# Kernel tuning notes

Measured on AMD Instinct MI355X. Metric: run time of the kernel, lower is better.

## Reference

```python
import jax, jax.numpy as jnp
import numpy as np

SUPPORT = 7
NEIGHBOR = 10
EPS = 1e-12
BN_EPS = 1e-5


def knn(v, k):
    # v: (b, n, 3) -> (b, n, k) indices of k nearest (excluding self)
    sq = jnp.sum(v * v, -1)
    d = sq[:, :, None] + sq[:, None, :] - 2.0 * jnp.einsum('bnd,bmd->bnm', v, v)
    _, idx = jax.lax.top_k(-d, k + 1)
    return idx[:, :, 1:]


def gather_nb(f, idx):
    # f: (b, n, c), idx: (b, m, k) -> (b, m, k, c)
    b = f.shape[0]
    return f[jnp.arange(b)[:, None, None], idx]


def nb_dir_norm(v, idx):
    d = gather_nb(v, idx) - v[:, :, None, :]
    n = jnp.linalg.norm(d, axis=-1, keepdims=True)
    return d / jnp.maximum(n, EPS)


def norm0(d):
    n = jnp.linalg.norm(d, axis=0, keepdims=True)
    return d / jnp.maximum(n, EPS)


def conv_surface(idx, v, directions, kernel_num):
    b, n, k = idx.shape
    dn = nb_dir_norm(v, idx)
    theta = jax.nn.relu(jnp.einsum('bnkd,de->bnke', dn, norm0(directions)))
    theta = theta.reshape(b, n, k, SUPPORT, kernel_num)
    return jnp.sum(jnp.max(theta, axis=2), axis=2)  # (b, n, kernel_num)


def conv_layer(idx, v, fmap, w, bias, directions, out_ch):
    b, n, k = idx.shape
    dn = nb_dir_norm(v, idx)
    theta = jax.nn.relu(jnp.einsum('bnkd,de->bnke', dn, norm0(directions)))  # (b,n,k,s*o)
    fout = fmap @ w + bias  # (b, n, (s+1)*o)
    center = fout[..., :out_ch]
    supp = gather_nb(fout[..., out_ch:], idx)  # (b, n, k, s*o)
    act = (theta * supp).reshape(b, n, k, SUPPORT, out_ch)
    return center + jnp.sum(jnp.max(act, axis=2), axis=2)


def pool(v, f, rate, nbn, seed):
    b, n, _ = v.shape
    idx = knn(v, nbn)
    pf = jnp.max(gather_nb(f, idx), axis=2)
    m = n // rate
    samp = jax.random.permutation(jax.random.key(seed), n)[:m]
    return v[:, samp, :], pf[:, samp, :]


def nearest_idx(tgt, src):
    d = (jnp.sum(src * src, -1)[:, None, :] + jnp.sum(tgt * tgt, -1)[:, :, None]
         - 2.0 * jnp.einsum('btd,bsd->bts', tgt, src))
    return jnp.argmin(d, axis=-1)  # (b, nt)


def bn(x, g, b_, m, var):
    # per-channel over last dim (torch BN1d after transpose)
    return (x - m) / jnp.sqrt(var + BN_EPS) * g + b_


def setup_inputs() -> dict:
    key = jax.random.key(0)
    ks = jax.random.split(key, 32)
    bs, n = 4, 2048
    d = {}
    d['vertices'] = jax.random.normal(ks[0], (bs, n, 3), jnp.float32)
    d['rgb_f'] = jax.random.normal(ks[1], (bs, 32, n), jnp.float32)
    d['dir0'] = jax.random.normal(ks[2], (3, SUPPORT * 64), jnp.float32)
    def conv_params(i, cin, cout):
        s = 1.0 / np.sqrt(cin)
        w = jax.random.uniform(ks[i], (cin, (SUPPORT + 1) * cout), jnp.float32, -s, s)
        b = jax.random.uniform(ks[i + 1], ((SUPPORT + 1) * cout,), jnp.float32, -s, s)
        dr = jax.random.normal(ks[i + 2], (3, SUPPORT * cout), jnp.float32)
        return w, b, dr
    d['w1'], d['b1'], d['d1'] = conv_params(3, 128, 128)
    d['w2'], d['b2'], d['d2'] = conv_params(6, 128, 256)
    d['w3'], d['b3'], d['d3'] = conv_params(9, 256, 256)
    d['w4'], d['b4'], d['d4'] = conv_params(12, 256, 512)
    d['rgb_w'] = jax.random.normal(ks[15], (64, 32), jnp.float32) * 0.1
    d['rgb_b'] = jnp.zeros((64,), jnp.float32)
    for nm, c in [('rbn', 64), ('bn1', 128), ('bn2', 256), ('bn3', 256)]:
        d[nm + '_g'] = jnp.ones((c,), jnp.float32)
        d[nm + '_b'] = jnp.zeros((c,), jnp.float32)
        d[nm + '_m'] = jnp.zeros((c,), jnp.float32)
        d[nm + '_v'] = jnp.ones((c,), jnp.float32)
    return d


def reference(vertices, rgb_f, dir0,
              w1, b1, d1, w2, b2, d2, w3, b3, d3, w4, b4, d4,
              rgb_w, rgb_b,
              rbn_g, rbn_b, rbn_m, rbn_v,
              bn1_g, bn1_b, bn1_m, bn1_v,
              bn2_g, bn2_b, bn2_m, bn2_v,
              bn3_g, bn3_b, bn3_m, bn3_v):
    bs, n, _ = vertices.shape
    idx = knn(vertices, NEIGHBOR)
    fm0 = jax.nn.relu(conv_surface(idx, vertices, dir0, 64))  # (b, n, 64)
    # rgb_conv_1: Conv1d(32,64,1) -> ReLU -> BN
    rgb = jax.nn.relu(jnp.einsum('oc,bcn->bno', rgb_w, rgb_f) + rgb_b)  # (b, n, 64)
    rgb = bn(rgb, rbn_g, rbn_b, rbn_m, rbn_v)
    fm0 = jnp.concatenate([fm0, rgb], axis=-1)  # (b, n, 128)
    fm1 = jax.nn.relu(bn(conv_layer(idx, vertices, fm0, w1, b1, d1, 128),
                         bn1_g, bn1_b, bn1_m, bn1_v))
    v1, fp1 = pool(vertices, fm1, 4, 4, 1)  # (b, n/4, ...)
    k1 = min(NEIGHBOR, v1.shape[1] // 8)
    idx1 = knn(v1, k1)
    fm2 = jax.nn.relu(bn(conv_layer(idx1, v1, fp1, w2, b2, d2, 256),
                         bn2_g, bn2_b, bn2_m, bn2_v))
    fm3 = jax.nn.relu(bn(conv_layer(idx1, v1, fm2, w3, b3, d3, 256),
                         bn3_g, bn3_b, bn3_m, bn3_v))
    v2, fp2 = pool(v1, fm3, 4, 4, 2)  # (b, n/16, ...)
    k2 = min(NEIGHBOR, v2.shape[1] // 8)
    idx2 = knn(v2, k2)
    fm4 = conv_layer(idx2, v2, fp2, w4, b4, d4, 512)
    f_global = jnp.max(fm4, axis=1)  # (b, 512)
    ni1 = nearest_idx(vertices, v1)  # (b, n)
    ni2 = nearest_idx(vertices, v2)
    ar = jnp.arange(bs)[:, None]
    fm2u = fm2[ar, ni1]
    fm3u = fm3[ar, ni1]
    fm4u = fm4[ar, ni2]
    feat = jnp.concatenate([fm0, fm1, fm2u, fm3u, fm4u], axis=2)  # (b, n, 1280)
    fuse = jnp.concatenate([feat, jnp.broadcast_to(f_global[:, None, :], (bs, n, 512))], axis=2)
    return feat.transpose(0, 2, 1), fuse.transpose(0, 2, 1)
```

## Files before the change

### kernel.cpp

```cpp
#include <hip/hip_runtime.h>
#include <hip/hip_bf16.h>
#include <math.h>

#define NB 10
#define KNN_K 11

typedef __attribute__((ext_vector_type(8))) short bf16x8;
typedef __attribute__((ext_vector_type(4))) float f32x4;
typedef unsigned long long ull;

__device__ __forceinline__ float toF(float x) { return x; }
__device__ __forceinline__ float toF(__hip_bfloat16 x) { return __bfloat162float(x); }

__device__ __forceinline__ void tf2x32(unsigned k0, unsigned k1, unsigned& x0, unsigned& x1) {
  unsigned ks0 = k0, ks1 = k1, ks2 = k0 ^ k1 ^ 0x1BD11BDAu;
  x0 += ks0; x1 += ks1;
#define TF_R(r) { x0 += x1; x1 = (x1 << (r)) | (x1 >> (32 - (r))); x1 ^= x0; }
  TF_R(13) TF_R(15) TF_R(26) TF_R(6)  x0 += ks1; x1 += ks2 + 1u;
  TF_R(17) TF_R(29) TF_R(16) TF_R(24) x0 += ks2; x1 += ks0 + 2u;
  TF_R(13) TF_R(15) TF_R(26) TF_R(6)  x0 += ks0; x1 += ks1 + 3u;
  TF_R(17) TF_R(29) TF_R(16) TF_R(24) x0 += ks1; x1 += ks2 + 4u;
  TF_R(13) TF_R(15) TF_R(26) TF_R(6)  x0 += ks2; x1 += ks0 + 5u;
#undef TF_R
}

template <int NITER>
__device__ __forceinline__ void knn_extract_body(const float4* __restrict__ pts, int qi,
                                                 int lane, int* __restrict__ o) {
  float4 p = pts[qi];
  float d[NITER];
#pragma unroll
  for (int i = 0; i < NITER; ++i) {
    float4 q = pts[lane + 64 * i];
    float dot = p.x * q.x + p.y * q.y + p.z * q.z;
    d[i] = p.w + q.w - 2.0f * dot;
  }
  unsigned mask = 0u;
#pragma unroll 1
  for (int t = 0; t < KNN_K; ++t) {
    float bestd = 3.4e38f; int besti = 0x7fffffff;
#pragma unroll
    for (int i = 0; i < NITER; ++i) {
      bool valid = ((mask >> i) & 1u) == 0u;
      bool better = valid && (d[i] < bestd);
      bestd = better ? d[i] : bestd;
      besti = better ? (lane + 64 * i) : besti;
    }
    float rd = bestd; int ridx = besti;
#pragma unroll
    for (int s = 32; s > 0; s >>= 1) {
      float od = __shfl_xor(rd, s);
      int oi = __shfl_xor(ridx, s);
      if (od < rd || (od == rd && oi < ridx)) { rd = od; ridx = oi; }
    }
    if ((ridx & 63) == lane) mask |= 1u << (ridx >> 6);
    if (t >= 1 && lane == 0) o[t - 1] = ridx;
  }
}

template <int NITER>
__global__ __launch_bounds__(1024) void knn_wave_kernel(const float* __restrict__ v,
                                                        int* __restrict__ out) {
  __shared__ float4 pts[NITER * 64];
  const int N = NITER * 64;
  int b = blockIdx.y;
  const float* vb = v + (size_t)b * N * 3;
  for (int i = threadIdx.x; i < N; i += blockDim.x) {
    float x = vb[i * 3], y = vb[i * 3 + 1], z = vb[i * 3 + 2];
    pts[i] = make_float4(x, y, z, x * x + y * y + z * z);
  }
  __syncthreads();
  int qpb = blockDim.x >> 6;
  int wave = threadIdx.x >> 6;
  int lane = threadIdx.x & 63;
  int qi = blockIdx.x * qpb + wave;
  knn_extract_body<NITER>(pts, qi, lane, out + ((size_t)b * N + qi) * NB);
}

__global__ __launch_bounds__(1024) void prep_kernel(
    const float* __restrict__ w1, __hip_bfloat16* __restrict__ o1,
    const float* __restrict__ w2, __hip_bfloat16* __restrict__ o2,
    const float* __restrict__ w3, __hip_bfloat16* __restrict__ o3,
    const float* __restrict__ w4, __hip_bfloat16* __restrict__ o4,
    const float* __restrict__ s0, float* __restrict__ n0,
    const float* __restrict__ s1, float* __restrict__ n1,
    const float* __restrict__ s2, float* __restrict__ n2,
    const float* __restrict__ s3, float* __restrict__ n3,
    const float* __restrict__ s4, float* __restrict__ n4,
    int* __restrict__ p1a, int* __restrict__ p1b, int* __restrict__ samp2) {
  __shared__ __align__(16) char smem[16896];
  int bid = blockIdx.x;
  if (bid < 480) {
    int sub = threadIdx.x >> 8, t = threadIdx.x & 255;
    int wtile = bid * 4 + sub;
    float (*tbuf)[33] = (float(*)[33])(smem + sub * (32 * 33 * 4));
    const float* W; __hip_bfloat16* O; int K, N;
    if (wtile < 128)      { W = w1; O = o1; K = 128; N = 1024; }
    else if (wtile < 384) { wtile -= 128; W = w2; O = o2; K = 128; N = 2048; }
    else if (wtile < 896) { wtile -= 384; W = w3; O = o3; K = 256; N = 2048; }
    else                  { wtile -= 896; W = w4; O = o4; K = 256; N = 4096; }
    int tpr = N / 32;
    int tk = wtile / tpr, tn = wtile % tpr;
    int tx = t & 31, ty = t >> 5;
#pragma unroll
    for (int i = 0; i < 4; ++i)
      tbuf[ty + 8 * i][tx] = W[(size_t)(tk * 32 + ty + 8 * i) * N + tn * 32 + tx];
    __syncthreads();
#pragma unroll
    for (int i = 0; i < 4; ++i)
      O[(size_t)(tn * 32 + ty + 8 * i) * K + tk * 32 + tx] = __float2bfloat16(tbuf[tx][ty + 8 * i]);
    return;
  }
  if (bid < 489) {
    int e = (bid - 480) * 1024 + threadIdx.x;
    const float* S; float* D; int W;
    if (e < 448)                          { S = s0; D = n0; W = 448; }
    else if (e < 448 + 896)               { e -= 448; S = s1; D = n1; W = 896; }
    else if (e < 448 + 896 + 1792)        { e -= 448 + 896; S = s2; D = n2; W = 1792; }
    else if (e < 448 + 896 + 3584)        { e -= 448 + 896 + 1792; S = s3; D = n3; W = 1792; }
    else if (e < 448 + 896 + 3584 + 3584) { e -= 448 + 896 + 3584; S = s4; D = n4; W = 3584; }
    else return;
    float a = S[e], b = S[W + e], c = S[2 * W + e];
    float nr = fmaxf(sqrtf(a * a + b * b + c * c), 1e-12f);
    D[e] = a / nr; D[W + e] = b / nr; D[2 * W + e] = c / nr;
    return;
  }
  {
    ull* keys = (ull*)smem;
    int which, chunk;
    if (bid < 497)      { which = 0; chunk = bid - 489; }
    else if (bid < 505) { which = 1; chunk = bid - 497; }
    else                { which = 2; chunk = 0; }
    unsigned mk0, mk1;
    if (which == 0)      { mk0 = 0u; mk1 = 1u; }
    else if (which == 1) { unsigned a0 = 0u, a1 = 0u; tf2x32(0u, 1u, a0, a1); mk0 = a0; mk1 = a1; }
    else                 { mk0 = 0u; mk1 = 2u; }
    unsigned sk0 = 0u, sk1 = 1u;
    tf2x32(mk0, mk1, sk0, sk1);
    int n = (which == 2) ? 512 : 2048;
    int* outp = (which == 0) ? p1a : (which == 1) ? p1b : samp2;
    for (int i = threadIdx.x; i < n; i += 1024) {
      unsigned y0 = 0u, y1 = (unsigned)i;
      tf2x32(sk0, sk1, y0, y1);
      keys[i] = ((ull)(y0 ^ y1) << 32) | (unsigned)i;
    }
    __syncthreads();
    int rpb = (which == 2) ? 512 : 256;
    int tpr = 1024 / rpb;
    int row = chunk * rpb + (int)(threadIdx.x / tpr);
    int sub = threadIdx.x % tpr;
    int seg = n / tpr;
    ull my = keys[row];
    int cnt = 0;
    for (int j = sub * seg; j < (sub + 1) * seg; ++j) cnt += (keys[j] < my) ? 1 : 0;
#pragma unroll
    for (int m = 1; m < 4; m <<= 1)
      if (m < tpr) cnt += __shfl_xor(cnt, m);
    if (sub == 0) outp[cnt] = row;
  }
}

__global__ __launch_bounds__(256) void fm0n_kernel(const float* __restrict__ v, const int* __restrict__ idx,
                                                   const float* __restrict__ dir0n,
                                                   const float* __restrict__ rgb_f, const float* __restrict__ w,
                                                   const float* __restrict__ bias, const float* __restrict__ g,
                                                   const float* __restrict__ bb, const float* __restrict__ mm,
                                                   const float* __restrict__ vv,
                                                   const int* __restrict__ p1a, const int* __restrict__ p1b,
                                                   const int* __restrict__ samp2,
                                                   float* __restrict__ fm0, __hip_bfloat16* __restrict__ fm0b,
                                                   int* __restrict__ ni1, int* __restrict__ ni2) {
  int z = blockIdx.z;
  int b = blockIdx.y;
  int tid = threadIdx.x;
  if (z >= 1) {
    __shared__ float4 sp[512];
    int S = (z == 1) ? 512 : 128;
    int* outp = (z == 1) ? ni1 : ni2;
    for (int i = tid; i < S; i += blockDim.x) {
      int src = (z == 1) ? p1a[p1b[i]] : p1a[p1b[samp2[i]]];
      const float* q = v + ((size_t)b * 2048 + src) * 3;
      float x = q[0], y = q[1], zz = q[2];
      sp[i] = make_float4(x, y, zz, x * x + y * y + zz * zz);
    }
    __syncthreads();
    int wave = tid >> 6, lane = tid & 63;
    int n = blockIdx.x * 4 + wave;
    const float* t = v + ((size_t)b * 2048 + n) * 3;
    float x = t[0], y = t[1], zz = t[2];
    float sqt = x * x + y * y + zz * zz;
    float best = 3.4e38f; int bi = 0x7fffffff;
    for (int s = lane; s < S; s += 64) {
      float4 q = sp[s];
      float d = q.w + sqt - 2.f * (x * q.x + y * q.y + zz * q.z);
      if (d < best) { best = d; bi = s; }
    }
#pragma unroll
    for (int m = 32; m > 0; m >>= 1) {
      float od = __shfl_xor(best, m);
      int oi = __shfl_xor(bi, m);
      if (od < best || (od == best && oi < bi)) { best = od; bi = oi; }
    }
    if (lane == 0) outp[(size_t)b * 2048 + n] = bi;
    return;
  }
  __shared__ float dn[4][NB][3];
  int n0 = blockIdx.x * 4;
  if (tid < 4 * NB) {
    int p = tid / NB, k = tid % NB;
    size_t row = (size_t)b * 2048 + (n0 + p);
    const float* c = v + row * 3;
    int nb = idx[row * NB + k];
    const float* q = v + ((size_t)b * 2048 + nb) * 3;
    float dx = q[0] - c[0], dy = q[1] - c[1], dz = q[2] - c[2];
    float nr = fmaxf(sqrtf(dx * dx + dy * dy + dz * dz), 1e-12f);
    dn[p][k][0] = dx / nr; dn[p][k][1] = dy / nr; dn[p][k][2] = dz / nr;
  }
  __syncthreads();
  int p = tid >> 6, c = tid & 63;
  int n = n0 + p;
  float acc = 0.f;
  for (int s = 0; s < 7; ++s) {
    int e = s * 64 + c;
    float d0 = dir0n[e], d1 = dir0n[448 + e], d2 = dir0n[896 + e];
    float mx = 0.f;
#pragma unroll
    for (int k = 0; k < NB; ++k) {
      float t = dn[p][k][0] * d0 + dn[p][k][1] * d1 + dn[p][k][2] * d2;
      mx = fmaxf(mx, fmaxf(t, 0.f));
    }
    acc += mx;
  }
  acc = fmaxf(acc, 0.f);
  const float* f = rgb_f + (size_t)b * 32 * 2048;
  float a2 = bias[c];
  for (int cc = 0; cc < 32; ++cc) a2 += w[c * 32 + cc] * f[cc * 2048 + n];
  a2 = fmaxf(a2, 0.f);
  a2 = (a2 - mm[c]) / sqrtf(vv[c] + 1e-5f) * g[c] + bb[c];
  size_t o = ((size_t)b * 2048 + n) * 128;
  fm0[o + c] = acc;
  fm0[o + 64 + c] = a2;
  fm0b[o + c] = __float2bfloat16(acc);
  fm0b[o + 64 + c] = __float2bfloat16(a2);
}

__global__ __launch_bounds__(256) void mfma_gemm_kernel(const __hip_bfloat16* __restrict__ A,
                                                        const __hip_bfloat16* __restrict__ BT,
                                                        const float* __restrict__ bias,
                                                        float* __restrict__ C,
                                                        __hip_bfloat16* __restrict__ Cb,
                                                        int M, int K, int N) {
  __shared__ __hip_bfloat16 Al[128 * 32];
  __shared__ __hip_bfloat16 Bl[128 * 32];
  int t = threadIdx.x;
  int l = t & 63;
  int w = t >> 6;
  int wm = w >> 1, wn = w & 1;
  int m0 = blockIdx.y * 128, n0 = blockIdx.x * 128;
  f32x4 zero = {0.f, 0.f, 0.f, 0.f};
  f32x4 acc[4][4];
#pragma unroll
  for (int i = 0; i < 4; ++i)
#pragma unroll
    for (int j = 0; j < 4; ++j) acc[i][j] = zero;

  for (int kt = 0; kt < K; kt += 32) {
#pragma unroll
    for (int j = 0; j < 2; ++j) {
      int c = t + 256 * j;
      int r = c >> 2, o = c & 3;
      *(uint4*)&Al[r * 32 + o * 8] = *(const uint4*)&A[(size_t)(m0 + r) * K + kt + o * 8];
      *(uint4*)&Bl[r * 32 + o * 8] = *(const uint4*)&BT[(size_t)(n0 + r) * K + kt + o * 8];
    }
    __syncthreads();
    bf16x8 af[4], bfv[4];
#pragma unroll
    for (int f = 0; f < 4; ++f) {
      af[f]  = *(const bf16x8*)&Al[(wm * 64 + f * 16 + (l & 15)) * 32 + (l >> 4) * 8];
      bfv[f] = *(const bf16x8*)&Bl[(wn * 64 + f * 16 + (l & 15)) * 32 + (l >> 4) * 8];
    }
#pragma unroll
    for (int i = 0; i < 4; ++i)
#pragma unroll
      for (int j = 0; j < 4; ++j)
        acc[i][j] = __builtin_amdgcn_mfma_f32_16x16x32_bf16(af[i], bfv[j], acc[i][j], 0, 0, 0);
    __syncthreads();
  }
  int col_l = l & 15, rbase = (l >> 4) * 4;
#pragma unroll
  for (int i = 0; i < 4; ++i) {
#pragma unroll
    for (int j = 0; j < 4; ++j) {
      int col = n0 + wn * 64 + j * 16 + col_l;
      float bv = bias[col];
#pragma unroll
      for (int r = 0; r < 4; ++r) {
        int m = m0 + wm * 64 + i * 16 + rbase + r;
        float val = acc[i][j][r] + bv;
        if (C)  C[(size_t)m * N + col] = val;
        if (Cb) Cb[(size_t)m * N + col] = __float2bfloat16(val);
      }
    }
  }
}

template <typename T>
__global__ __launch_bounds__(256) void conv_combine3_kernel(
    const int* __restrict__ idx, const float* __restrict__ v,
    const T* __restrict__ fout, const float* __restrict__ dirn,
    const float* __restrict__ g, const float* __restrict__ bb,
    const float* __restrict__ mm, const float* __restrict__ vv,
    int use_bn_relu, float* __restrict__ outf, __hip_bfloat16* __restrict__ outb,
    int Np, int Cout) {
  __shared__ float dnS[2][NB][3];
  __shared__ int nbS[2][NB];
  int b = blockIdx.y;
  int tid = threadIdx.x;
  int base = blockIdx.x * 256;
  int p0 = base / Cout;
  int nPts = (Cout < 256) ? 2 : 1;
  if (tid < nPts * NB) {
    int p = tid / NB, k = tid - p * NB;
    size_t prow = (size_t)b * Np + p0 + p;
    int nb = idx[prow * NB + k];
    const float* cpt = v + prow * 3;
    const float* q = v + ((size_t)b * Np + nb) * 3;
    float dx = q[0] - cpt[0], dy = q[1] - cpt[1], dz = q[2] - cpt[2];
    float nr = fmaxf(sqrtf(dx * dx + dy * dy + dz * dz), 1e-12f);
    dnS[p][k][0] = dx / nr; dnS[p][k][1] = dy / nr; dnS[p][k][2] = dz / nr;
    nbS[p][k] = b * Np + nb;
  }
  __syncthreads();
  int gid = base + tid;
  int n = gid / Cout, c = gid - n * Cout;
  int lp = n - p0;
  size_t row = (size_t)b * Np + n;
  float dn0[NB], dn1[NB], dn2[NB]; int nbr[NB];
#pragma unroll
  for (int k = 0; k < NB; ++k) {
    dn0[k] = dnS[lp][k][0]; dn1[k] = dnS[lp][k][1]; dn2[k] = dnS[lp][k][2];
    nbr[k] = nbS[lp][k];
  }
  int F = 8 * Cout, W7 = 7 * Cout;
  float acc = toF(fout[row * (size_t)F + c]);
  for (int s = 0; s < 7; ++s) {
    int e = s * Cout + c;
    float d0 = dirn[e], d1 = dirn[W7 + e], d2 = dirn[2 * W7 + e];
    float mx = -3.4e38f;
#pragma unroll
    for (int k = 0; k < NB; ++k) {
      float t = fmaxf(dn0[k] * d0 + dn1[k] * d1 + dn2[k] * d2, 0.f);
      float sv = toF(fout[(size_t)nbr[k] * F + Cout + e]);
      mx = fmaxf(mx, t * sv);
    }
    acc += mx;
  }
  if (use_bn_relu) {
    acc = (acc - mm[c]) / sqrtf(vv[c] + 1e-5f) * g[c] + bb[c];
    acc = fmaxf(acc, 0.f);
  }
  outf[row * (size_t)Cout + c] = acc;
  if (outb) outb[row * (size_t)Cout + c] = __float2bfloat16(acc);
}

__global__ void pool_kernel(const float* __restrict__ v, const float* __restrict__ fm,
                            const int* __restrict__ idx10,
                            const int* __restrict__ sampA, const int* __restrict__ sampB,
                            float* __restrict__ v_out, float* __restrict__ f_out,
                            __hip_bfloat16* __restrict__ f_out_b, int Nin, int C) {
  int b = blockIdx.y, mi = blockIdx.x, c = threadIdx.x;
  int n = sampB ? sampA[sampB[mi]] : sampA[mi];
  size_t row = (size_t)b * Nin + n;
  float mx = -3.4e38f;
#pragma unroll
  for (int j = 0; j < 4; ++j) {
    int nb = idx10[row * NB + j];
    mx = fmaxf(mx, fm[((size_t)b * Nin + nb) * C + c]);
  }
  int Mout = gridDim.x;
  f_out[((size_t)b * Mout + mi) * C + c] = mx;
  f_out_b[((size_t)b * Mout + mi) * C + c] = __float2bfloat16(mx);
  if (c < 3) v_out[((size_t)b * Mout + mi) * 3 + c] = v[row * 3 + c];
}

__global__ __launch_bounds__(256) void output3_kernel(
    const float* __restrict__ fm0, const float* __restrict__ fm1,
    const float* __restrict__ fm2, const float* __restrict__ fm3,
    const float* __restrict__ fm4,
    const int* __restrict__ ni1, const int* __restrict__ ni2,
    float* __restrict__ out) {
  __shared__ float tile[64][33];
  __shared__ int srow[64];
  int b = blockIdx.z;
  int cc0 = blockIdx.y * 32;
  int n0 = blockIdx.x * 64;
  int tid = threadIdx.x;
  float* out0 = out;
  float* out1 = out + (size_t)4 * 1280 * 2048;
  if (cc0 >= 1280) {
    __shared__ float red[8][32];
    __shared__ float fgv[32];
    int coff = cc0 - 1280;
    int tx = tid & 31, ty = tid >> 5;
    float pm = -3.4e38f;
    for (int p = ty; p < 128; p += 8)
      pm = fmaxf(pm, fm4[((size_t)b * 128 + p) * 512 + coff + tx]);
    red[ty][tx] = pm;
    __syncthreads();
    if (tid < 32) {
      float m = red[0][tid];
#pragma unroll
      for (int r = 1; r < 8; ++r) m = fmaxf(m, red[r][tid]);
      fgv[tid] = m;
    }
    __syncthreads();
    int lx = tid & 63, ly = tid >> 6;
#pragma unroll
    for (int ci = 0; ci < 8; ++ci) {
      int cl = ly + 4 * ci;
      out1[((size_t)b * 1792 + cc0 + cl) * 2048 + n0 + lx] = fgv[cl];
    }
    return;
  }
  const float* P; int Cs, coff, mode;
  if (cc0 < 128)       { P = fm0; Cs = 128; coff = cc0;        mode = 0; }
  else if (cc0 < 256)  { P = fm1; Cs = 128; coff = cc0 - 128;  mode = 0; }
  else if (cc0 < 512)  { P = fm2; Cs = 256; coff = cc0 - 256;  mode = 1; }
  else if (cc0 < 768)  { P = fm3; Cs = 256; coff = cc0 - 512;  mode = 1; }
  else                 { P = fm4; Cs = 512; coff = cc0 - 768;  mode = 2; }
  if (tid < 64) {
    int n = n0 + tid;
    size_t r2 = (size_t)b * 2048 + n;
    int sr;
    if (mode == 0)      sr = b * 2048 + n;
    else if (mode == 1) sr = b * 512 + ni1[r2];
    else                sr = b * 128 + ni2[r2];
    srow[tid] = sr;
  }
  __syncthreads();
  int tx = tid & 31, ty = tid >> 5;
#pragma unroll
  for (int r = 0; r < 8; ++r) {
    int nl = ty + 8 * r;
    tile[nl][tx] = P[(size_t)srow[nl] * Cs + coff + tx];
  }
  __syncthreads();
  int lx = tid & 63, ly = tid >> 6;
#pragma unroll
  for (int ci = 0; ci < 8; ++ci) {
    int cl = ly + 4 * ci;
    int cc = cc0 + cl;
    float vv = tile[lx][cl];
    out1[((size_t)b * 1792 + cc) * 2048 + n0 + lx] = vv;
    out0[((size_t)b * 1280 + cc) * 2048 + n0 + lx] = vv;
  }
}

extern "C" void kernel_launch(void* const* d_in, const int* in_sizes, int n_in,
                              void* d_out, int out_size, void* d_ws, size_t ws_size,
                              hipStream_t stream) {
  (void)in_sizes; (void)n_in; (void)out_size; (void)ws_size;
  const float* vertices = (const float*)d_in[0];
  const float* rgb_f    = (const float*)d_in[1];
  const float* dir0     = (const float*)d_in[2];
  const float* w1 = (const float*)d_in[3],  *b1 = (const float*)d_in[4],  *d1 = (const float*)d_in[5];
  const float* w2 = (const float*)d_in[6],  *b2 = (const float*)d_in[7],  *d2 = (const float*)d_in[8];
  const float* w3 = (const float*)d_in[9],  *b3 = (const float*)d_in[10], *d3 = (const float*)d_in[11];
  const float* w4 = (const float*)d_in[12], *b4 = (const float*)d_in[13], *d4 = (const float*)d_in[14];
  const float* rgb_w = (const float*)d_in[15], *rgb_b = (const float*)d_in[16];
  const float* rbn_g = (const float*)d_in[17], *rbn_b = (const float*)d_in[18];
  const float* rbn_m = (const float*)d_in[19], *rbn_v = (const float*)d_in[20];
  const float* bn1_g = (const float*)d_in[21], *bn1_b = (const float*)d_in[22];
  const float* bn1_m = (const float*)d_in[23], *bn1_v = (const float*)d_in[24];
  const float* bn2_g = (const float*)d_in[25], *bn2_b = (const float*)d_in[26];
  const float* bn2_m = (const float*)d_in[27], *bn2_v = (const float*)d_in[28];
  const float* bn3_g = (const float*)d_in[29], *bn3_b = (const float*)d_in[30];
  const float* bn3_m = (const float*)d_in[31], *bn3_v = (const float*)d_in[32];
  float* out = (float*)d_out;

  char* ws = (char*)d_ws;
  size_t off = 0;
  auto alloc = [&](size_t bytes) -> void* {
    void* p = ws + off;
    off += (bytes + 255) & ~(size_t)255;
    return p;
  };
  int*   p1a   = (int*)alloc(2048 * 4);
  int*   p1b   = (int*)alloc(2048 * 4);
  int*   samp2 = (int*)alloc(512 * 4);
  int*   idx0  = (int*)alloc((size_t)4 * 2048 * NB * 4);
  int*   idx1  = (int*)alloc((size_t)4 * 512 * NB * 4);
  int*   idx2  = (int*)alloc((size_t)4 * 128 * NB * 4);
  float* fm0   = (float*)alloc((size_t)4 * 2048 * 128 * 4);
  float* fm1   = (float*)alloc((size_t)4 * 2048 * 128 * 4);
  float* fout  = (float*)alloc((size_t)4 * 2048 * 1024 * 4);
  __hip_bfloat16* foutb = (__hip_bfloat16*)alloc((size_t)4 * 2048 * 1024 * 2);
  float* v1    = (float*)alloc((size_t)4 * 512 * 3 * 4);
  float* fp1   = (float*)alloc((size_t)4 * 512 * 128 * 4);
  float* fm2   = (float*)alloc((size_t)4 * 512 * 256 * 4);
  float* fm3   = (float*)alloc((size_t)4 * 512 * 256 * 4);
  float* v2    = (float*)alloc((size_t)4 * 128 * 3 * 4);
  float* fp2   = (float*)alloc((size_t)4 * 128 * 256 * 4);
  float* fm4   = (float*)alloc((size_t)4 * 128 * 512 * 4);
  int*   ni1   = (int*)alloc((size_t)4 * 2048 * 4);
  int*   ni2   = (int*)alloc((size_t)4 * 2048 * 4);
  __hip_bfloat16* fm0b = (__hip_bfloat16*)alloc((size_t)4 * 2048 * 128 * 2);
  __hip_bfloat16* fp1b = (__hip_bfloat16*)alloc((size_t)4 * 512 * 128 * 2);
  __hip_bfloat16* fm2b = (__hip_bfloat16*)alloc((size_t)4 * 512 * 256 * 2);
  __hip_bfloat16* fp2b = (__hip_bfloat16*)alloc((size_t)4 * 128 * 256 * 2);
  __hip_bfloat16* wt1  = (__hip_bfloat16*)alloc((size_t)1024 * 128 * 2);
  __hip_bfloat16* wt2  = (__hip_bfloat16*)alloc((size_t)2048 * 128 * 2);
  __hip_bfloat16* wt3  = (__hip_bfloat16*)alloc((size_t)2048 * 256 * 2);
  __hip_bfloat16* wt4  = (__hip_bfloat16*)alloc((size_t)4096 * 256 * 2);
  float* d0n = (float*)alloc((size_t)3 * 448 * 4);
  float* d1n = (float*)alloc((size_t)3 * 896 * 4);
  float* d2n = (float*)alloc((size_t)3 * 1792 * 4);
  float* d3n = (float*)alloc((size_t)3 * 1792 * 4);
  float* d4n = (float*)alloc((size_t)3 * 3584 * 4);

  prep_kernel<<<506, 1024, 0, stream>>>(w1, wt1, w2, wt2, w3, wt3, w4, wt4,
                                        dir0, d0n, d1, d1n, d2, d2n, d3, d3n, d4, d4n,
                                        p1a, p1b, samp2);

  knn_wave_kernel<32><<<dim3(128, 4), 1024, 0, stream>>>(vertices, idx0);

  fm0n_kernel<<<dim3(512, 4, 3), 256, 0, stream>>>(vertices, idx0, d0n, rgb_f, rgb_w, rgb_b,
                                                   rbn_g, rbn_b, rbn_m, rbn_v, p1a, p1b, samp2,
                                                   fm0, fm0b, ni1, ni2);

  mfma_gemm_kernel<<<dim3(1024 / 128, 8192 / 128), 256, 0, stream>>>(fm0b, wt1, b1, nullptr, foutb, 8192, 128, 1024);
  conv_combine3_kernel<__hip_bfloat16><<<dim3(2048 * 128 / 256, 4), 256, 0, stream>>>(idx0, vertices, foutb, d1n,
      bn1_g, bn1_b, bn1_m, bn1_v, 1, fm1, nullptr, 2048, 128);

  pool_kernel<<<dim3(512, 4), 128, 0, stream>>>(vertices, fm1, idx0, p1a, p1b, v1, fp1, fp1b, 2048, 128);
  knn_wave_kernel<8><<<dim3(128, 4), 256, 0, stream>>>(v1, idx1);

  mfma_gemm_kernel<<<dim3(2048 / 128, 2048 / 128), 256, 0, stream>>>(fp1b, wt2, b2, nullptr, foutb, 2048, 128, 2048);
  conv_combine3_kernel<__hip_bfloat16><<<dim3(512 * 256 / 256, 4), 256, 0, stream>>>(idx1, v1, foutb, d2n,
      bn2_g, bn2_b, bn2_m, bn2_v, 1, fm2, fm2b, 512, 256);
  mfma_gemm_kernel<<<dim3(2048 / 128, 2048 / 128), 256, 0, stream>>>(fm2b, wt3, b3, nullptr, foutb, 2048, 256, 2048);
  conv_combine3_kernel<__hip_bfloat16><<<dim3(512 * 256 / 256, 4), 256, 0, stream>>>(idx1, v1, foutb, d3n,
      bn3_g, bn3_b, bn3_m, bn3_v, 1, fm3, nullptr, 512, 256);

  pool_kernel<<<dim3(128, 4), 256, 0, stream>>>(v1, fm3, idx1, samp2, nullptr, v2, fp2, fp2b, 512, 256);
  knn_wave_kernel<2><<<dim3(32, 4), 256, 0, stream>>>(v2, idx2);

  mfma_gemm_kernel<<<dim3(4096 / 128, 512 / 128), 256, 0, stream>>>(fp2b, wt4, b4, fout, nullptr, 512, 256, 4096);
  conv_combine3_kernel<float><<<dim3(128 * 512 / 256, 4), 256, 0, stream>>>(idx2, v2, fout, d4n,
      nullptr, nullptr, nullptr, nullptr, 0, fm4, nullptr, 128, 512);

  output3_kernel<<<dim3(32, 56, 4), 256, 0, stream>>>(fm0, fm1, fm2, fm3, fm4, ni1, ni2, out);
}
```

Measured before the change: 252.6 us.

## Replace wave-per-query KNN with thread-per-query split top-k and merge

The first-level KNN over 2048 points used to run one wavefront per query, doing 11 rounds of wave-wide argmin shuffles. It now runs one thread per query: each thread keeps a register insertion-sorted top-11 over a 256-point slice, and a second kernel merges the 8 partial lists per query. The partial results are staged in the existing fout scratch buffer, and the launch adds one extra kernel. Separately, the permutation-rank part of the prep kernel is spread over more blocks, with fewer rows per block and more threads counting each row, to raise parallelism.

```diff
diff --git a/kernel.cpp b/kernel.cpp
--- a/kernel.cpp
+++ b/kernel.cpp
@@ -24,6 +24,74 @@
 #undef TF_R
 }
 
+#define KNN_INSERT(cd_, ci_)                                 \
+  {                                                          \
+    float cdv_ = (cd_); int civ_ = (ci_);                    \
+    _Pragma("unroll")                                        \
+    for (int t_ = 0; t_ < KNN_K; ++t_) {                     \
+      bool sw_ = cdv_ < bd[t_];                              \
+      float td_ = bd[t_]; int ti_ = bi[t_];                  \
+      bd[t_] = sw_ ? cdv_ : td_; bi[t_] = sw_ ? civ_ : ti_;  \
+      cdv_ = sw_ ? td_ : cdv_;   civ_ = sw_ ? ti_ : civ_;    \
+    }                                                        \
+  }
+
+__global__ __launch_bounds__(256) void knn0_part_kernel(const float* __restrict__ v,
+                                                        float* __restrict__ partd,
+                                                        int* __restrict__ parti) {
+  __shared__ float4 pts[256];
+  int b = blockIdx.z, sl = blockIdx.y, qb = blockIdx.x;
+  const float* vb = v + (size_t)b * 2048 * 3;
+  int c0 = sl * 256;
+  {
+    int j = c0 + threadIdx.x;
+    float x = vb[j * 3], y = vb[j * 3 + 1], z = vb[j * 3 + 2];
+    pts[threadIdx.x] = make_float4(x, y, z, x * x + y * y + z * z);
+  }
+  __syncthreads();
+  int q = qb * 256 + threadIdx.x;
+  float px = vb[q * 3], py = vb[q * 3 + 1], pz = vb[q * 3 + 2];
+  float pw = px * px + py * py + pz * pz;
+  float bd[KNN_K]; int bi[KNN_K];
+#pragma unroll
+  for (int t = 0; t < KNN_K; ++t) { bd[t] = 3.4e38f; bi[t] = 0x7fffffff; }
+  for (int i = 0; i < 256; ++i) {
+    float4 qq = pts[i];
+    float dot = px * qq.x + py * qq.y + pz * qq.z;
+    float d = pw + qq.w - 2.0f * dot;
+    if (d < bd[KNN_K - 1]) KNN_INSERT(d, c0 + i);
+  }
+  size_t base = ((size_t)(b * 8 + sl) * KNN_K) * 2048 + q;
+#pragma unroll
+  for (int k = 0; k < KNN_K; ++k) {
+    partd[base + (size_t)k * 2048] = bd[k];
+    parti[base + (size_t)k * 2048] = bi[k];
+  }
+}
+
+__global__ __launch_bounds__(256) void knn0_merge_kernel(const float* __restrict__ partd,
+                                                         const int* __restrict__ parti,
+                                                         int* __restrict__ idx0) {
+  int b = blockIdx.y;
+  int q = blockIdx.x * 256 + threadIdx.x;
+  float bd[KNN_K]; int bi[KNN_K];
+#pragma unroll
+  for (int t = 0; t < KNN_K; ++t) { bd[t] = 3.4e38f; bi[t] = 0x7fffffff; }
+  for (int s = 0; s < 8; ++s) {
+    for (int k = 0; k < KNN_K; ++k) {
+      size_t base = ((size_t)(b * 8 + s) * KNN_K + k) * 2048 + q;
+      float cd = partd[base];
+      if (cd < bd[KNN_K - 1]) {
+        int ci = parti[base];
+        KNN_INSERT(cd, ci);
+      } else break;
+    }
+  }
+  int* o = idx0 + ((size_t)b * 2048 + q) * NB;
+#pragma unroll
+  for (int t = 1; t < KNN_K; ++t) o[t - 1] = bi[t];
+}
+
 template <int NITER>
 __device__ __forceinline__ void knn_extract_body(const float4* __restrict__ pts, int qi,
                                                  int lane, int* __restrict__ o) {
@@ -59,8 +127,7 @@
 }
 
 template <int NITER>
-__global__ __launch_bounds__(1024) void knn_wave_kernel(const float* __restrict__ v,
-                                                        int* __restrict__ out) {
+__global__ void knn_wave_kernel(const float* __restrict__ v, int* __restrict__ out) {
   __shared__ float4 pts[NITER * 64];
   const int N = NITER * 64;
   int b = blockIdx.y;
@@ -128,8 +195,8 @@
   {
     ull* keys = (ull*)smem;
     int which, chunk;
-    if (bid < 497)      { which = 0; chunk = bid - 489; }
-    else if (bid < 505) { which = 1; chunk = bid - 497; }
+    if (bid < 521)      { which = 0; chunk = bid - 489; }
+    else if (bid < 553) { which = 1; chunk = bid - 521; }
     else                { which = 2; chunk = 0; }
     unsigned mk0, mk1;
     if (which == 0)      { mk0 = 0u; mk1 = 1u; }
@@ -145,7 +212,7 @@
       keys[i] = ((ull)(y0 ^ y1) << 32) | (unsigned)i;
     }
     __syncthreads();
-    int rpb = (which == 2) ? 512 : 256;
+    int rpb = (which == 2) ? 512 : 64;
     int tpr = 1024 / rpb;
     int row = chunk * rpb + (int)(threadIdx.x / tpr);
     int sub = threadIdx.x % tpr;
@@ -154,7 +221,7 @@
     int cnt = 0;
     for (int j = sub * seg; j < (sub + 1) * seg; ++j) cnt += (keys[j] < my) ? 1 : 0;
 #pragma unroll
-    for (int m = 1; m < 4; m <<= 1)
+    for (int m = 1; m < 16; m <<= 1)
       if (m < tpr) cnt += __shfl_xor(cnt, m);
     if (sub == 0) outp[cnt] = row;
   }
@@ -518,11 +585,15 @@
   float* d3n = (float*)alloc((size_t)3 * 1792 * 4);
   float* d4n = (float*)alloc((size_t)3 * 3584 * 4);
 
-  prep_kernel<<<506, 1024, 0, stream>>>(w1, wt1, w2, wt2, w3, wt3, w4, wt4,
+  float* partd = fout;
+  int*   parti = (int*)(fout + 720896);
+
+  prep_kernel<<<554, 1024, 0, stream>>>(w1, wt1, w2, wt2, w3, wt3, w4, wt4,
                                         dir0, d0n, d1, d1n, d2, d2n, d3, d3n, d4, d4n,
                                         p1a, p1b, samp2);
 
-  knn_wave_kernel<32><<<dim3(128, 4), 1024, 0, stream>>>(vertices, idx0);
+  knn0_part_kernel<<<dim3(8, 8, 4), 256, 0, stream>>>(vertices, partd, parti);
+  knn0_merge_kernel<<<dim3(8, 4), 256, 0, stream>>>(partd, parti, idx0);
 
   fm0n_kernel<<<dim3(512, 4, 3), 256, 0, stream>>>(vertices, idx0, d0n, rgb_f, rgb_w, rgb_b,
                                                    rbn_g, rbn_b, rbn_m, rbn_v, p1a, p1b, samp2,
```

Result: slower. 406.1 us (+60.7%).

## Replace wave-per-query KNN with thread-per-query insertion sort and split-merge

Applied to the files above, without the earlier changes.

The wave-per-query KNN, which ran 11 rounds of wave reductions, is replaced by a per-thread register top-11 insertion sort. The large level-0 KNN is split across 16 candidate slices with partial results written to scratch memory that aliases fout, then merged in a second kernel. The small levels use a single thread-per-query kernel. The permutation-rank part of prep_kernel is also spread over more blocks (64 rows per block instead of 256). Risks include very low parallelism in knn_small (2 and 1 blocks per batch), divergence in the insert branch, and tie-breaking that may differ from top_k.

```diff
diff --git a/kernel.cpp b/kernel.cpp
--- a/kernel.cpp
+++ b/kernel.cpp
@@ -24,45 +24,78 @@
 #undef TF_R
 }
 
-template <int NITER>
-__device__ __forceinline__ void knn_extract_body(const float4* __restrict__ pts, int qi,
-                                                 int lane, int* __restrict__ o) {
-  float4 p = pts[qi];
-  float d[NITER];
-#pragma unroll
-  for (int i = 0; i < NITER; ++i) {
-    float4 q = pts[lane + 64 * i];
-    float dot = p.x * q.x + p.y * q.y + p.z * q.z;
-    d[i] = p.w + q.w - 2.0f * dot;
-  }
-  unsigned mask = 0u;
-#pragma unroll 1
-  for (int t = 0; t < KNN_K; ++t) {
-    float bestd = 3.4e38f; int besti = 0x7fffffff;
-#pragma unroll
-    for (int i = 0; i < NITER; ++i) {
-      bool valid = ((mask >> i) & 1u) == 0u;
-      bool better = valid && (d[i] < bestd);
-      bestd = better ? d[i] : bestd;
-      besti = better ? (lane + 64 * i) : besti;
-    }
-    float rd = bestd; int ridx = besti;
-#pragma unroll
-    for (int s = 32; s > 0; s >>= 1) {
-      float od = __shfl_xor(rd, s);
-      int oi = __shfl_xor(ridx, s);
-      if (od < rd || (od == rd && oi < ridx)) { rd = od; ridx = oi; }
-    }
-    if ((ridx & 63) == lane) mask |= 1u << (ridx >> 6);
-    if (t >= 1 && lane == 0) o[t - 1] = ridx;
-  }
-}
-
-template <int NITER>
-__global__ __launch_bounds__(1024) void knn_wave_kernel(const float* __restrict__ v,
+#define KNN_DECL                                                        \
+  float d0=3.4e38f,d1=3.4e38f,d2=3.4e38f,d3=3.4e38f,d4=3.4e38f,         \
+        d5=3.4e38f,d6=3.4e38f,d7=3.4e38f,d8=3.4e38f,d9=3.4e38f,d10=3.4e38f; \
+  int   i0=0x7fffffff,i1=0x7fffffff,i2=0x7fffffff,i3=0x7fffffff,        \
+        i4=0x7fffffff,i5=0x7fffffff,i6=0x7fffffff,i7=0x7fffffff,        \
+        i8=0x7fffffff,i9=0x7fffffff,i10=0x7fffffff;
+
+#define KNN_SLOT(K)                                                     \
+  { bool sw_ = cdv_ < d##K; float td_ = d##K; int ti_ = i##K;           \
+    d##K = sw_ ? cdv_ : td_; i##K = sw_ ? civ_ : ti_;                   \
+    cdv_ = sw_ ? td_ : cdv_; civ_ = sw_ ? ti_ : civ_; }
+
+#define KNN_INSERT_S(cd_, ci_)                                          \
+  { float cdv_ = (cd_); int civ_ = (ci_);                               \
+    KNN_SLOT(0) KNN_SLOT(1) KNN_SLOT(2) KNN_SLOT(3) KNN_SLOT(4)        \
+    KNN_SLOT(5) KNN_SLOT(6) KNN_SLOT(7) KNN_SLOT(8) KNN_SLOT(9)        \
+    KNN_SLOT(10) }
+
+__global__ __launch_bounds__(256) void knn0_part_kernel(const float* __restrict__ v,
+                                                        float* __restrict__ partd,
+                                                        int* __restrict__ parti) {
+  __shared__ float4 pts[128];
+  int b = blockIdx.z, sl = blockIdx.y, qb = blockIdx.x;
+  const float* vb = v + (size_t)b * 2048 * 3;
+  int c0 = sl * 128;
+  if (threadIdx.x < 128) {
+    int j = c0 + threadIdx.x;
+    float x = vb[j * 3], y = vb[j * 3 + 1], z = vb[j * 3 + 2];
+    pts[threadIdx.x] = make_float4(x, y, z, x * x + y * y + z * z);
+  }
+  __syncthreads();
+  int q = qb * 256 + threadIdx.x;
+  float px = vb[q * 3], py = vb[q * 3 + 1], pz = vb[q * 3 + 2];
+  float pw = px * px + py * py + pz * pz;
+  KNN_DECL
+  for (int i = 0; i < 128; ++i) {
+    float4 qq = pts[i];
+    float dot = px * qq.x + py * qq.y + pz * qq.z;
+    float d = pw + qq.w - 2.0f * dot;
+    if (d < d10) KNN_INSERT_S(d, c0 + i);
+  }
+  size_t base = ((size_t)(b * 16 + sl) * KNN_K) * 2048 + q;
+#define KNN_STORE(K) { partd[base + (size_t)K * 2048] = d##K; parti[base + (size_t)K * 2048] = i##K; }
+  KNN_STORE(0) KNN_STORE(1) KNN_STORE(2) KNN_STORE(3) KNN_STORE(4)
+  KNN_STORE(5) KNN_STORE(6) KNN_STORE(7) KNN_STORE(8) KNN_STORE(9) KNN_STORE(10)
+#undef KNN_STORE
+}
+
+__global__ __launch_bounds__(256) void knn0_merge_kernel(const float* __restrict__ partd,
+                                                         const int* __restrict__ parti,
+                                                         int* __restrict__ idx0) {
+  int b = blockIdx.y;
+  int q = blockIdx.x * 256 + threadIdx.x;
+  KNN_DECL
+  for (int s = 0; s < 16; ++s) {
+    for (int k = 0; k < KNN_K; ++k) {
+      size_t base = ((size_t)(b * 16 + s) * KNN_K + k) * 2048 + q;
+      float cd = partd[base];
+      if (cd < d10) {
+        int ci = parti[base];
+        KNN_INSERT_S(cd, ci);
+      } else break;
+    }
+  }
+  int* o = idx0 + ((size_t)b * 2048 + q) * NB;
+  o[0] = i1; o[1] = i2; o[2] = i3; o[3] = i4; o[4] = i5;
+  o[5] = i6; o[6] = i7; o[7] = i8; o[8] = i9; o[9] = i10;
+}
+
+__global__ __launch_bounds__(256) void knn_small_kernel(const float* __restrict__ v, int N,
                                                         int* __restrict__ out) {
-  __shared__ float4 pts[NITER * 64];
-  const int N = NITER * 64;
+  __shared__ float4 pts[512];
   int b = blockIdx.y;
   const float* vb = v + (size_t)b * N * 3;
   for (int i = threadIdx.x; i < N; i += blockDim.x) {
@@ -70,11 +103,19 @@
     pts[i] = make_float4(x, y, z, x * x + y * y + z * z);
   }
   __syncthreads();
-  int qpb = blockDim.x >> 6;
-  int wave = threadIdx.x >> 6;
-  int lane = threadIdx.x & 63;
-  int qi = blockIdx.x * qpb + wave;
-  knn_extract_body<NITER>(pts, qi, lane, out + ((size_t)b * N + qi) * NB);
+  int q = blockIdx.x * 256 + threadIdx.x;
+  if (q >= N) return;
+  float4 p = pts[q];
+  KNN_DECL
+  for (int i = 0; i < N; ++i) {
+    float4 qq = pts[i];
+    float dot = p.x * qq.x + p.y * qq.y + p.z * qq.z;
+    float d = p.w + qq.w - 2.0f * dot;
+    if (d < d10) KNN_INSERT_S(d, i);
+  }
+  int* o = out + ((size_t)b * N + q) * NB;
+  o[0] = i1; o[1] = i2; o[2] = i3; o[3] = i4; o[4] = i5;
+  o[5] = i6; o[6] = i7; o[7] = i8; o[8] = i9; o[9] = i10;
 }
 
 __global__ __launch_bounds__(1024) void prep_kernel(
@@ -128,8 +169,8 @@
   {
     ull* keys = (ull*)smem;
     int which, chunk;
-    if (bid < 497)      { which = 0; chunk = bid - 489; }
-    else if (bid < 505) { which = 1; chunk = bid - 497; }
+    if (bid < 521)      { which = 0; chunk = bid - 489; }
+    else if (bid < 553) { which = 1; chunk = bid - 521; }
     else                { which = 2; chunk = 0; }
     unsigned mk0, mk1;
     if (which == 0)      { mk0 = 0u; mk1 = 1u; }
@@ -145,7 +186,7 @@
       keys[i] = ((ull)(y0 ^ y1) << 32) | (unsigned)i;
     }
     __syncthreads();
-    int rpb = (which == 2) ? 512 : 256;
+    int rpb = (which == 2) ? 512 : 64;
     int tpr = 1024 / rpb;
     int row = chunk * rpb + (int)(threadIdx.x / tpr);
     int sub = threadIdx.x % tpr;
@@ -154,7 +195,7 @@
     int cnt = 0;
     for (int j = sub * seg; j < (sub + 1) * seg; ++j) cnt += (keys[j] < my) ? 1 : 0;
 #pragma unroll
-    for (int m = 1; m < 4; m <<= 1)
+    for (int m = 1; m < 16; m <<= 1)
       if (m < tpr) cnt += __shfl_xor(cnt, m);
     if (sub == 0) outp[cnt] = row;
   }
@@ -222,11 +263,11 @@
   float acc = 0.f;
   for (int s = 0; s < 7; ++s) {
     int e = s * 64 + c;
-    float d0 = dir0n[e], d1 = dir0n[448 + e], d2 = dir0n[896 + e];
+    float dd0 = dir0n[e], dd1 = dir0n[448 + e], dd2 = dir0n[896 + e];
     float mx = 0.f;
 #pragma unroll
     for (int k = 0; k < NB; ++k) {
-      float t = dn[p][k][0] * d0 + dn[p][k][1] * d1 + dn[p][k][2] * d2;
+      float t = dn[p][k][0] * dd0 + dn[p][k][1] * dd1 + dn[p][k][2] * dd2;
       mx = fmaxf(mx, fmaxf(t, 0.f));
     }
     acc += mx;
@@ -345,11 +386,11 @@
   float acc = toF(fout[row * (size_t)F + c]);
   for (int s = 0; s < 7; ++s) {
     int e = s * Cout + c;
-    float d0 = dirn[e], d1 = dirn[W7 + e], d2 = dirn[2 * W7 + e];
+    float e0 = dirn[e], e1 = dirn[W7 + e], e2 = dirn[2 * W7 + e];
     float mx = -3.4e38f;
 #pragma unroll
     for (int k = 0; k < NB; ++k) {
-      float t = fmaxf(dn0[k] * d0 + dn1[k] * d1 + dn2[k] * d2, 0.f);
+      float t = fmaxf(dn0[k] * e0 + dn1[k] * e1 + dn2[k] * e2, 0.f);
       float sv = toF(fout[(size_t)nbr[k] * F + Cout + e]);
       mx = fmaxf(mx, t * sv);
     }
@@ -518,11 +559,15 @@
   float* d3n = (float*)alloc((size_t)3 * 1792 * 4);
   float* d4n = (float*)alloc((size_t)3 * 3584 * 4);
 
-  prep_kernel<<<506, 1024, 0, stream>>>(w1, wt1, w2, wt2, w3, wt3, w4, wt4,
+  float* partd = fout;
+  int*   parti = (int*)(fout + 1441792);
+
+  prep_kernel<<<554, 1024, 0, stream>>>(w1, wt1, w2, wt2, w3, wt3, w4, wt4,
                                         dir0, d0n, d1, d1n, d2, d2n, d3, d3n, d4, d4n,
                                         p1a, p1b, samp2);
 
-  knn_wave_kernel<32><<<dim3(128, 4), 1024, 0, stream>>>(vertices, idx0);
+  knn0_part_kernel<<<dim3(8, 16, 4), 256, 0, stream>>>(vertices, partd, parti);
+  knn0_merge_kernel<<<dim3(8, 4), 256, 0, stream>>>(partd, parti, idx0);
 
   fm0n_kernel<<<dim3(512, 4, 3), 256, 0, stream>>>(vertices, idx0, d0n, rgb_f, rgb_w, rgb_b,
                                                    rbn_g, rbn_b, rbn_m, rbn_v, p1a, p1b, samp2,
@@ -533,7 +578,7 @@
       bn1_g, bn1_b, bn1_m, bn1_v, 1, fm1, nullptr, 2048, 128);
 
   pool_kernel<<<dim3(512, 4), 128, 0, stream>>>(vertices, fm1, idx0, p1a, p1b, v1, fp1, fp1b, 2048, 128);
-  knn_wave_kernel<8><<<dim3(128, 4), 256, 0, stream>>>(v1, idx1);
+  knn_small_kernel<<<dim3(2, 4), 256, 0, stream>>>(v1, 512, idx1);
 
   mfma_gemm_kernel<<<dim3(2048 / 128, 2048 / 128), 256, 0, stream>>>(fp1b, wt2, b2, nullptr, foutb, 2048, 128, 2048);
   conv_combine3_kernel<__hip_bfloat16><<<dim3(512 * 256 / 256, 4), 256, 0, stream>>>(idx1, v1, foutb, d2n,
@@ -543,7 +588,7 @@
       bn3_g, bn3_b, bn3_m, bn3_v, 1, fm3, nullptr, 512, 256);
 
   pool_kernel<<<dim3(128, 4), 256, 0, stream>>>(v1, fm3, idx1, samp2, nullptr, v2, fp2, fp2b, 512, 256);
-  knn_wave_kernel<2><<<dim3(32, 4), 256, 0, stream>>>(v2, idx2);
+  knn_small_kernel<<<dim3(1, 4), 256, 0, stream>>>(v2, 128, idx2);
 
   mfma_gemm_kernel<<<dim3(4096 / 128, 512 / 128), 256, 0, stream>>>(fp2b, wt4, b4, fout, nullptr, 512, 256, 4096);
   conv_combine3_kernel<float><<<dim3(128 * 512 / 256, 4), 256, 0, stream>>>(idx2, v2, fout, d4n,
```

New measurement: 633.9 us. +150.9%, slower.
